# Kernel tuning notes

Measured on AMD Instinct MI355X. Metric: run time of the kernel, lower is better.

The kernel has to match this reference:

```python
import jax, jax.numpy as jnp
import numpy as np

GROUPS = 32
EPS = 1e-6


def group_norm(x, gamma, beta):
    b, c, h, w = x.shape
    xg = x.reshape(b, GROUPS, c // GROUPS, h, w)
    mean = xg.mean(axis=(2, 3, 4), keepdims=True)
    var = xg.var(axis=(2, 3, 4), keepdims=True)
    xn = (xg - mean) * jax.lax.rsqrt(var + EPS)
    xn = xn.reshape(b, c, h, w)
    return xn * gamma[None, :, None, None] + beta[None, :, None, None]


def conv1x1(x, w, b):
    # x: [B,C,H,W], w: [O,C], b: [O]
    return jnp.einsum('bchw,oc->bohw', x, w) + b[None, :, None, None]


def setup_inputs() -> dict:
    key = jax.random.key(0)
    ks = jax.random.split(key, 6)
    C = 512
    B, H, W = 2, 64, 64
    s = (C) ** -0.5  # fan-in style init scale for 1x1 convs
    return {
        'x': jax.random.normal(ks[0], (B, C, H, W), jnp.float32),
        'gn_gamma': jnp.ones((C,), jnp.float32),
        'gn_beta': jnp.zeros((C,), jnp.float32),
        'wq': jax.random.normal(ks[1], (C, C), jnp.float32) * s,
        'bq': jnp.zeros((C,), jnp.float32),
        'wk': jax.random.normal(ks[2], (C, C), jnp.float32) * s,
        'bk': jnp.zeros((C,), jnp.float32),
        'wv': jax.random.normal(ks[3], (C, C), jnp.float32) * s,
        'bv': jnp.zeros((C,), jnp.float32),
        'wo': jax.random.normal(ks[4], (C, C), jnp.float32) * s,
        'bo': jnp.zeros((C,), jnp.float32),
    }


def reference(x, gn_gamma, gn_beta, wq, bq, wk, bk, wv, bv, wo, bo):
    b, c, h, w = x.shape
    n = h * w
    h_ = group_norm(x, gn_gamma, gn_beta)
    q = conv1x1(h_, wq, bq).reshape(b, c, n)   # [B,C,N]
    k = conv1x1(h_, wk, bk).reshape(b, c, n)   # [B,C,N]
    v = conv1x1(h_, wv, bv).reshape(b, c, n)   # [B,C,N]
    scale = jnp.asarray(int(c) ** (-0.5), x.dtype)
    # scores[b, nq, nk] = sum_c q[b,c,nq] * k[b,c,nk]
    scores = jnp.einsum('bcn,bcm->bnm', q, k) * scale
    attn = jax.nn.softmax(scores, axis=2)      # softmax over keys
    # out[b,c,nq] = sum_m v[b,c,m] * attn[b,nq,m]
    out = jnp.einsum('bcm,bnm->bcn', v, attn).reshape(b, c, h, w)
    out = conv1x1(out, wo, bo)
    return x + out
```

## Files before the change

kernel.cpp:

```cpp
#include <hip/hip_runtime.h>

typedef unsigned short u16;
typedef __attribute__((ext_vector_type(8))) unsigned short ushort8;
typedef __attribute__((ext_vector_type(8))) short bf16x8;
typedef __attribute__((ext_vector_type(4))) float f32x4;

#define DEVINL __device__ __forceinline__

DEVINL float bf2f(u16 u){ union{unsigned i; float f;} v; v.i = ((unsigned)u) << 16; return v.f; }
DEVINL u16 f2bf(float f){
  unsigned x = __builtin_bit_cast(unsigned, f);
  x += 0x7fffu + ((x >> 16) & 1u);
  return (u16)(x >> 16);
}
DEVINL void gl_lds16(const void* g, void* l){
  __builtin_amdgcn_global_load_lds((const __attribute__((address_space(1))) unsigned*)g,
                                   (__attribute__((address_space(3))) unsigned*)l, 16, 0, 0);
}
template<int N> DEVINL void wait_vmcnt(){
  asm volatile("s_waitcnt vmcnt(%0)" :: "n"(N) : "memory");
}
DEVINL void hard_barrier(){
  asm volatile("" ::: "memory");
  __builtin_amdgcn_s_barrier();
  asm volatile("" ::: "memory");
}
DEVINL float wsum(float v){
  #pragma unroll
  for (int o = 32; o; o >>= 1) v += __shfl_xor(v, o, 64);
  return v;
}

__global__ __launch_bounds__(256) void cvt4b_k(const float* __restrict__ s0, const float* __restrict__ s1,
                 const float* __restrict__ s2, const float* __restrict__ s3,
                 const float* __restrict__ bq, const float* __restrict__ bk, const float* __restrict__ bv,
                 u16* __restrict__ wdst, float* __restrict__ bdst){
  if (blockIdx.x == 512){
    for (int j = threadIdx.x; j < 1536; j += 256)
      bdst[j] = (j < 512) ? bq[j] : (j < 1024) ? bk[j-512] : bv[j-1024];
    return;
  }
  const int g = blockIdx.x >> 7;
  const float* src = (g==0) ? s0 : (g==1) ? s1 : (g==2) ? s2 : s3;
  const int i = ((blockIdx.x & 127)*256 + threadIdx.x)*8;
  float4 f0 = *(const float4*)(src + i);
  float4 f1 = *(const float4*)(src + i + 4);
  ushort8 o;
  o[0]=f2bf(f0.x); o[1]=f2bf(f0.y); o[2]=f2bf(f0.z); o[3]=f2bf(f0.w);
  o[4]=f2bf(f1.x); o[5]=f2bf(f1.y); o[6]=f2bf(f1.z); o[7]=f2bf(f1.w);
  *(ushort8*)(wdst + g*262144 + i) = o;
}

__global__ __launch_bounds__(256) void reduce4_k(const u16* __restrict__ part,
                 const float* __restrict__ psum, u16* __restrict__ dst){
  __shared__ float invsh[4];
  const int t = threadIdx.x, w = t>>6, ln = t&63;
  const int row = blockIdx.x*4 + w;
  float s = psum[ln*8192 + blockIdx.y*4096 + row];
  s = wsum(s);
  if (ln == 0) invsh[w] = 1.f / s;
  __syncthreads();
  const int i = (blockIdx.x*256 + t)*8;
  const u16* p = part + (size_t)blockIdx.y*8388608;
  float a[8] = {};
  #pragma unroll
  for (int ks = 0; ks < 4; ++ks){
    ushort8 u = *(const ushort8*)(p + (size_t)ks*2097152 + i);
    #pragma unroll
    for (int j = 0; j < 8; ++j) a[j] += bf2f(u[j]);
  }
  const float iv = invsh[w];
  ushort8 o;
  #pragma unroll
  for (int j = 0; j < 8; ++j) o[j] = f2bf(a[j] * iv);
  *(ushort8*)(dst + (size_t)blockIdx.y*2097152 + i) = o;
}

__global__ __launch_bounds__(256) void gn_stats_k(const float* __restrict__ x, float* __restrict__ stats){
  __shared__ __align__(16) float red[8];
  const float* px = x + ((size_t)blockIdx.x << 16);
  const int t = threadIdx.x;
  float s = 0.f, ss = 0.f;
  for (int off = t*4; off < 65536; off += 1024){
    float4 u = *(const float4*)(px + off);
    s  += u.x + u.y + u.z + u.w;
    ss += u.x*u.x + u.y*u.y + u.z*u.z + u.w*u.w;
  }
  s = wsum(s); ss = wsum(ss);
  if ((t & 63) == 0){ red[t>>6] = s; red[4+(t>>6)] = ss; }
  __syncthreads();
  if (t == 0){
    float S1 = red[0]+red[1]+red[2]+red[3];
    float S2 = red[4]+red[5]+red[6]+red[7];
    float mean = S1 * (1.f/65536.f);
    float var  = S2 * (1.f/65536.f) - mean*mean;
    stats[2*blockIdx.x]   = mean;
    stats[2*blockIdx.x+1] = rsqrtf(var + 1e-6f);
  }
}

__global__ __launch_bounds__(256) void gn_apply_k(const float* __restrict__ x, const float* __restrict__ gamma,
                 const float* __restrict__ beta, const float* __restrict__ stats, u16* __restrict__ ht){
  __shared__ __align__(16) u16 tile[32*512];
  const int b = blockIdx.y, n0 = blockIdx.x*32, t = threadIdx.x;
  #pragma unroll
  for (int it = 0; it < 8; ++it){
    int c  = it*64 + (t>>2);
    int nn = (t&3)*8;
    const float* px = x + ((size_t)(b*512 + c) << 12) + n0 + nn;
    float4 u0 = *(const float4*)(px);
    float4 u1 = *(const float4*)(px + 4);
    float mean = stats[2*(b*32 + (c>>4))];
    float rstd = stats[2*(b*32 + (c>>4)) + 1];
    float ga = gamma[c], be = beta[c];
    float f[8] = {u0.x,u0.y,u0.z,u0.w,u1.x,u1.y,u1.z,u1.w};
    #pragma unroll
    for (int j = 0; j < 8; ++j)
      tile[(nn+j)*512 + c] = f2bf((f[j] - mean) * rstd * ga + be);
  }
  __syncthreads();
  const int rw = t>>3, sg = t&7;
  #pragma unroll
  for (int uu = 0; uu < 8; ++uu){
    ushort8 v = *(const ushort8*)(tile + rw*512 + sg*64 + uu*8);
    *(ushort8*)(ht + ((size_t)(b*4096 + n0 + rw) << 9) + sg*64 + uu*8) = v;
  }
}

template<bool EXPSUM>
__global__ __launch_bounds__(512) void gemm8_nt(
    const u16* __restrict__ A, const u16* __restrict__ Bt, u16* __restrict__ C,
    float* __restrict__ psum,
    int K, int lda, int ldb, int ldc, int zdiv,
    long long aStrB, long long aStr, long long bStrB, long long bStr,
    long long cStrB, long long cStr)
{
  extern __shared__ __align__(16) char smem[];
  const int z = blockIdx.z, z1 = z / zdiv, z2 = z % zdiv;
  A  += (size_t)aStrB*z1 + (size_t)aStr*z2;
  Bt += (size_t)bStrB*z1 + (size_t)bStr*z2;
  C  += (size_t)cStrB*z1 + (size_t)cStr*z2;
  const int nwg = gridDim.x*gridDim.y;
  int wg = blockIdx.y*gridDim.x + blockIdx.x;
  wg = (wg & 7)*(nwg >> 3) + (wg >> 3);
  const int m0 = (wg / gridDim.x)*256, n0 = (wg % gridDim.x)*256;

  const int t = threadIdx.x, wv = t>>6, ln = t&63;
  const int wm = wv>>2, wn = wv&3;
  const int lq = ln&15, lg = ln>>4;
  const int srow = ln>>2;
  const int sseg = (((ln&3) ^ ((srow>>1)&3)))*8;
  const int rslot = (lg ^ ((lq>>1)&3))*16;

  auto STAGE_A = [&](int u){
    char* base = smem + (u&3)*16384 + wv*1024;
    const u16* g = A + (size_t)(m0 + wv*16 + srow)*lda + u*32 + sseg;
    gl_lds16(g, base);
    gl_lds16(g + (size_t)128*lda, base + 8192);
  };
  auto STAGE_B = [&](int u){
    char* base = smem + 65536 + (u&3)*16384 + wv*1024;
    const u16* g = Bt + (size_t)(n0 + wv*16 + srow)*ldb + u*32 + sseg;
    gl_lds16(g, base);
    gl_lds16(g + (size_t)128*ldb, base + 8192);
  };
  auto LDA4 = [&](int u, int mh, bf16x8* a){
    const char* p = smem + (u&3)*16384 + (wm*128 + mh*64 + lq)*64 + rslot;
    #pragma unroll
    for (int i = 0; i < 4; ++i) a[i] = *(const bf16x8*)(p + i*1024);
  };
  auto LDB4 = [&](int u, bf16x8* b){
    const char* p = smem + 65536 + (u&3)*16384 + (wn*64 + lq)*64 + rslot;
    #pragma unroll
    for (int j = 0; j < 4; ++j) b[j] = *(const bf16x8*)(p + j*1024);
  };

  f32x4 acc[8][4] = {};
  auto MFMA16 = [&](bf16x8* a4, bf16x8* b4, int moff){
    __builtin_amdgcn_s_setprio(1);
    #pragma unroll
    for (int n = 0; n < 4; ++n)
      #pragma unroll
      for (int m = 0; m < 4; ++m)
        acc[moff+m][n] = __builtin_amdgcn_mfma_f32_16x16x32_bf16(a4[m], b4[n], acc[moff+m][n], 0, 0, 0);
    __builtin_amdgcn_s_setprio(0);
  };

  STAGE_A(0); STAGE_B(0); STAGE_A(1); STAGE_B(1); STAGE_A(2); STAGE_B(2);
  wait_vmcnt<8>();
  hard_barrier();
  const int T = K >> 6;
  for (int tt = 0; tt < T; ++tt){
    const int u0 = 2*tt, u1 = 2*tt + 1;
    bf16x8 a[4], b[4];
    LDA4(u0, 0, a); LDB4(u0, b);
    if (tt < T-1) STAGE_A(u0+3);
    hard_barrier();
    MFMA16(a, b, 0);
    hard_barrier();
    LDA4(u0, 1, a);
    if (tt < T-1) STAGE_B(u0+3);
    if (tt == T-1) wait_vmcnt<0>(); else wait_vmcnt<8>();
    hard_barrier();
    MFMA16(a, b, 4);
    hard_barrier();
    LDA4(u1, 0, a); LDB4(u1, b);
    if (tt < T-2) STAGE_A(u0+4);
    hard_barrier();
    MFMA16(a, b, 0);
    hard_barrier();
    LDA4(u1, 1, a);
    if (tt < T-2) STAGE_B(u0+4);
    if (tt == T-2)      wait_vmcnt<4>();
    else if (tt < T-2)  wait_vmcnt<8>();
    hard_barrier();
    MFMA16(a, b, 4);
    hard_barrier();
  }
  const int slice = EXPSUM ? ((n0 >> 8)*4 + wn) : 0;
  #pragma unroll
  for (int m = 0; m < 8; ++m)
    #pragma unroll
    for (int r2 = 0; r2 < 4; ++r2){
      const int mg = m0 + wm*128 + m*16 + lg*4 + r2;
      u16* cp = C + (size_t)mg*ldc + n0 + wn*64 + lq;
      if constexpr (EXPSUM){
        float e[4], rs = 0.f;
        #pragma unroll
        for (int n = 0; n < 4; ++n){ e[n] = __expf(acc[m][n][r2]); rs += e[n]; }
        rs += __shfl_xor(rs, 1, 64);
        rs += __shfl_xor(rs, 2, 64);
        rs += __shfl_xor(rs, 4, 64);
        rs += __shfl_xor(rs, 8, 64);
        if (lq == 0) psum[slice*8192 + z1*4096 + mg] = rs;
        #pragma unroll
        for (int n = 0; n < 4; ++n) cp[n*16] = f2bf(e[n]);
      } else {
        #pragma unroll
        for (int n = 0; n < 4; ++n) cp[n*16] = f2bf(acc[m][n][r2]);
      }
    }
}

__global__ __launch_bounds__(256) void qkv_k(
    const u16* __restrict__ Wstk, const u16* __restrict__ ht,
    const float* __restrict__ biases, u16* __restrict__ dstBase)
{
  __shared__ __align__(16) char smem[32768];
  char* smA0 = smem;
  char* smA1 = smem + 8192;
  char* smB0 = smem + 16384;
  char* smB1 = smem + 24576;
  const int z = blockIdx.z, mat = z >> 1, b = z & 1;
  const u16* A  = Wstk + mat*262144;
  const u16* Bt = ht + (size_t)b*2097152;
  const float* bias = biases + mat*512;
  const float oscale = (mat == 0) ? 0.044194173824159216f : 1.0f;
  u16* dst = dstBase + (size_t)mat*4194304 + (size_t)b*2097152;
  const int m0 = blockIdx.y*128, n0 = blockIdx.x*128;
  const int t = threadIdx.x, wv = t>>6, ln = t&63;
  const int wm = wv>>1, wn = wv&1;
  const int lq = ln&15, lg = ln>>4;
  const int srow = ln>>2;
  const int sseg = (((ln&3) ^ ((srow>>1)&3)))*8;
  const int rslot = (lg ^ ((lq>>1)&3))*16;
  f32x4 acc[4][4] = {};
  for (int kk = 0; kk < 512; kk += 64){
    __syncthreads();
    #pragma unroll
    for (int r = 0; r < 2; ++r){
      const int rr = r*64 + wv*16;
      const u16* pa = A  + (size_t)(m0 + rr + srow)*512 + kk + sseg;
      const u16* pb = Bt + (size_t)(n0 + rr + srow)*512 + kk + sseg;
      gl_lds16(pa,      smA0 + rr*64);
      gl_lds16(pa + 32, smA1 + rr*64);
      gl_lds16(pb,      smB0 + rr*64);
      gl_lds16(pb + 32, smB1 + rr*64);
    }
    __syncthreads();
    #pragma unroll
    for (int half = 0; half < 2; ++half){
      const char* pA = half ? smA1 : smA0;
      const char* pB = half ? smB1 : smB0;
      bf16x8 af[4], bfv[4];
      #pragma unroll
      for (int i = 0; i < 4; ++i) af[i]  = *(const bf16x8*)(pA + ((wm*64 + i*16 + lq)<<6) + rslot);
      #pragma unroll
      for (int j = 0; j < 4; ++j) bfv[j] = *(const bf16x8*)(pB + ((wn*64 + j*16 + lq)<<6) + rslot);
      #pragma unroll
      for (int i = 0; i < 4; ++i)
        #pragma unroll
        for (int j = 0; j < 4; ++j)
          acc[i][j] = __builtin_amdgcn_mfma_f32_16x16x32_bf16(af[i], bfv[j], acc[i][j], 0, 0, 0);
    }
  }
  if (mat == 2){
    #pragma unroll
    for (int i = 0; i < 4; ++i)
      #pragma unroll
      for (int r2 = 0; r2 < 4; ++r2){
        const int mg = m0 + wm*64 + i*16 + lg*4 + r2;
        float bv = bias[mg];
        #pragma unroll
        for (int j = 0; j < 4; ++j){
          const int ng = n0 + wn*64 + j*16 + lq;
          dst[(size_t)mg*4096 + ng] = f2bf(acc[i][j][r2] + bv);
        }
      }
  } else {
    __syncthreads();
    u16* ct = (u16*)smem;
    #pragma unroll
    for (int i = 0; i < 4; ++i)
      #pragma unroll
      for (int j = 0; j < 4; ++j)
        #pragma unroll
        for (int r2 = 0; r2 < 4; ++r2){
          const int ml = wm*64 + i*16 + lg*4 + r2;
          const int nl = wn*64 + j*16 + lq;
          ct[nl*128 + ml] = f2bf((acc[i][j][r2] + bias[m0 + ml]) * oscale);
        }
    __syncthreads();
    const int rw = t>>1, hf = (t&1)*64;
    #pragma unroll
    for (int u = 0; u < 8; ++u){
      *(ushort8*)(dst + (size_t)(n0 + rw)*512 + m0 + hf + u*8) =
          *(const ushort8*)(ct + rw*128 + hf + u*8);
    }
  }
}

template<bool TRANS_OUT, bool HAS_BIAS, bool HAS_RES, bool F32OUT>
__global__ __launch_bounds__(256) void gemm_nt(
    const u16* __restrict__ A, const u16* __restrict__ Bt,
    const float* __restrict__ bias, const float* __restrict__ res, void* __restrict__ Cw_,
    int K, int lda, int ldb, int ldc, int zdiv,
    long long aStrB, long long aStr, long long bStrB, long long bStr,
    long long cStrB, long long cStr, long long rStrB, float oscale)
{
  __shared__ __align__(16) char smem[32768];
  char* smA0 = smem;
  char* smA1 = smem + 8192;
  char* smB0 = smem + 16384;
  char* smB1 = smem + 24576;
  const int z = blockIdx.z;
  const int z1 = z / zdiv, z2 = z % zdiv;
  A  += (size_t)aStrB*z1 + (size_t)aStr*z2;
  Bt += (size_t)bStrB*z1 + (size_t)bStr*z2;
  u16*   Cw16 = (u16*)Cw_   + (size_t)cStrB*z1 + (size_t)cStr*z2;
  float* Cw32 = (float*)Cw_ + (size_t)cStrB*z1 + (size_t)cStr*z2;
  const float* resp = HAS_RES ? (res + (size_t)rStrB*z1) : nullptr;
  const int m0 = blockIdx.y*128, n0 = blockIdx.x*128;
  const int t = threadIdx.x, wv = t>>6, ln = t&63;
  const int wm = wv>>1, wn = wv&1;
  const int lq = ln&15, lg = ln>>4;
  const int srow = ln>>2;
  const int sseg = (((ln&3) ^ ((srow>>1)&3)))*8;
  const int rslot = (lg ^ ((lq>>1)&3))*16;
  f32x4 acc[4][4] = {};
  for (int kk = 0; kk < K; kk += 64){
    __syncthreads();
    #pragma unroll
    for (int r = 0; r < 2; ++r){
      const int rr = r*64 + wv*16;
      const u16* pa = A  + (size_t)(m0 + rr + srow)*lda + kk + sseg;
      const u16* pb = Bt + (size_t)(n0 + rr + srow)*ldb + kk + sseg;
      gl_lds16(pa,      smA0 + rr*64);
      gl_lds16(pa + 32, smA1 + rr*64);
      gl_lds16(pb,      smB0 + rr*64);
      gl_lds16(pb + 32, smB1 + rr*64);
    }
    __syncthreads();
    #pragma unroll
    for (int half = 0; half < 2; ++half){
      const char* pA = half ? smA1 : smA0;
      const char* pB = half ? smB1 : smB0;
      bf16x8 af[4], bfv[4];
      #pragma unroll
      for (int i = 0; i < 4; ++i) af[i]  = *(const bf16x8*)(pA + ((wm*64 + i*16 + lq)<<6) + rslot);
      #pragma unroll
      for (int j = 0; j < 4; ++j) bfv[j] = *(const bf16x8*)(pB + ((wn*64 + j*16 + lq)<<6) + rslot);
      #pragma unroll
      for (int i = 0; i < 4; ++i)
        #pragma unroll
        for (int j = 0; j < 4; ++j)
          acc[i][j] = __builtin_amdgcn_mfma_f32_16x16x32_bf16(af[i], bfv[j], acc[i][j], 0, 0, 0);
    }
  }
  if constexpr (!TRANS_OUT){
    #pragma unroll
    for (int i = 0; i < 4; ++i){
      #pragma unroll
      for (int r2 = 0; r2 < 4; ++r2){
        const int mg = m0 + wm*64 + i*16 + lg*4 + r2;
        float bv = HAS_BIAS ? bias[mg] : 0.f;
        #pragma unroll
        for (int j = 0; j < 4; ++j){
          const int ng = n0 + wn*64 + j*16 + lq;
          float v = (acc[i][j][r2] + bv) * oscale;
          if (HAS_RES) v += resp[(size_t)mg*ldc + ng];
          if constexpr (F32OUT) Cw32[(size_t)mg*ldc + ng] = v;
          else                  Cw16[(size_t)mg*ldc + ng] = f2bf(v);
        }
      }
    }
  } else {
    __syncthreads();
    u16* ct = (u16*)smem;
    #pragma unroll
    for (int i = 0; i < 4; ++i)
      #pragma unroll
      for (int j = 0; j < 4; ++j)
        #pragma unroll
        for (int r2 = 0; r2 < 4; ++r2){
          const int ml = wm*64 + i*16 + lg*4 + r2;
          const int nl = wn*64 + j*16 + lq;
          float v = acc[i][j][r2];
          if (HAS_BIAS) v += bias[m0 + ml];
          ct[nl*128 + ml] = f2bf(v * oscale);
        }
    __syncthreads();
    const int rw = t>>1, hf = (t&1)*64;
    #pragma unroll
    for (int u = 0; u < 8; ++u){
      *(ushort8*)(Cw16 + (size_t)(n0 + rw)*ldc + m0 + hf + u*8) =
          *(const ushort8*)(ct + rw*128 + hf + u*8);
    }
  }
}

extern "C" void kernel_launch(void* const* d_in, const int* in_sizes, int n_in,
                              void* d_out, int out_size, void* d_ws, size_t ws_size,
                              hipStream_t stream)
{
  const float* x   = (const float*)d_in[0];
  const float* gam = (const float*)d_in[1];
  const float* bet = (const float*)d_in[2];
  const float* wq  = (const float*)d_in[3];
  const float* bq  = (const float*)d_in[4];
  const float* wk  = (const float*)d_in[5];
  const float* bk  = (const float*)d_in[6];
  const float* wvp = (const float*)d_in[7];
  const float* bv  = (const float*)d_in[8];
  const float* wo  = (const float*)d_in[9];
  const float* bo  = (const float*)d_in[10];
  float* out = (float*)d_out;

  char* w = (char*)d_ws;
  float* stats   = (float*)w;
  float* psum    = (float*)(w + 4096);
  float* biasQKV = (float*)(w + 2134016);
  u16* wqb  = (u16*)(w + (size_t)4194304);
  u16* wob  = wqb + 3*262144;
  u16* Qt   = wqb + 4*262144;
  u16* Kt   = Qt + 4194304;
  u16* Vb   = Kt + 4194304;
  u16* attT = Vb + 4194304;
  u16* Sbuf = attT + 4194304;
  u16* part = Sbuf + 33554432;
  u16* ht   = (u16*)d_out;

  const long long NC = 4096LL*512, NN = 4096LL*4096;

  cvt4b_k<<<dim3(513), dim3(256), 0, stream>>>(wq, wk, wvp, wo, bq, bk, bv, wqb, biasQKV);
  gn_stats_k<<<dim3(64), dim3(256), 0, stream>>>(x, stats);
  gn_apply_k<<<dim3(128,2), dim3(256), 0, stream>>>(x, gam, bet, stats, ht);
  qkv_k<<<dim3(32,4,6), dim3(256), 0, stream>>>(wqb, ht, biasQKV, Qt);
  gemm8_nt<true><<<dim3(16,16,2), dim3(512), 131072, stream>>>(
      Qt, Kt, Sbuf, psum, 512, 512, 512, 4096, 1, NC, 0, NC, 0, NN, 0);
  gemm8_nt<false><<<dim3(2,16,8), dim3(512), 131072, stream>>>(
      Sbuf, Vb, part, nullptr, 1024, 4096, 4096, 512, 4,
      NN, 1024, NC, 1024, 8388608, 2097152);
  reduce4_k<<<dim3(1024,2), dim3(256), 0, stream>>>(part, psum, attT);
  gemm_nt<false, true, true, true><<<dim3(32,4,2), dim3(256), 0, stream>>>(
      wob, attT, bo, x, out, 512, 512, 512, 4096, 1, 0,0, NC,0, NC,0, NC, 1.0f);
}
```

Measured before the change: 187.1 us.

## Shrink GEMM LDS to double buffering and split PV GEMM K eight ways

The 256x256 bf16 GEMM drops its 4-stage LDS ring and hand-scheduled two-step loop in favour of a 2-stage double buffer with a simple per-k-step loop, halving dynamic LDS from 128KB to 64KB. With less LDS per block, two blocks could fit per CU. The attention-times-V GEMM now splits K into 8 chunks of 512 instead of 4 of 1024, doubling its grid, and the reduction kernel sums 8 bf16 partials. The trade-off is less prefetch depth with a full vmcnt(0) wait every step, plus double the partial-buffer traffic and an extra bf16 rounding stage in the reduction.

New measurement: 197.4 us. 1.06x slower.

```diff
diff --git a/kernel.cpp b/kernel.cpp
--- a/kernel.cpp
+++ b/kernel.cpp
@@ -51,7 +51,7 @@
   *(ushort8*)(wdst + g*262144 + i) = o;
 }
 
-__global__ __launch_bounds__(256) void reduce4_k(const u16* __restrict__ part,
+__global__ __launch_bounds__(256) void reduce8_k(const u16* __restrict__ part,
                  const float* __restrict__ psum, u16* __restrict__ dst){
   __shared__ float invsh[4];
   const int t = threadIdx.x, w = t>>6, ln = t&63;
@@ -61,10 +61,10 @@
   if (ln == 0) invsh[w] = 1.f / s;
   __syncthreads();
   const int i = (blockIdx.x*256 + t)*8;
-  const u16* p = part + (size_t)blockIdx.y*8388608;
+  const u16* p = part + (size_t)blockIdx.y*16777216;
   float a[8] = {};
   #pragma unroll
-  for (int ks = 0; ks < 4; ++ks){
+  for (int ks = 0; ks < 8; ++ks){
     ushort8 u = *(const ushort8*)(p + (size_t)ks*2097152 + i);
     #pragma unroll
     for (int j = 0; j < 8; ++j) a[j] += bf2f(u[j]);
@@ -153,24 +153,24 @@
   const int rslot = (lg ^ ((lq>>1)&3))*16;
 
   auto STAGE_A = [&](int u){
-    char* base = smem + (u&3)*16384 + wv*1024;
+    char* base = smem + (u&1)*16384 + wv*1024;
     const u16* g = A + (size_t)(m0 + wv*16 + srow)*lda + u*32 + sseg;
     gl_lds16(g, base);
     gl_lds16(g + (size_t)128*lda, base + 8192);
   };
   auto STAGE_B = [&](int u){
-    char* base = smem + 65536 + (u&3)*16384 + wv*1024;
+    char* base = smem + 32768 + (u&1)*16384 + wv*1024;
     const u16* g = Bt + (size_t)(n0 + wv*16 + srow)*ldb + u*32 + sseg;
     gl_lds16(g, base);
     gl_lds16(g + (size_t)128*ldb, base + 8192);
   };
   auto LDA4 = [&](int u, int mh, bf16x8* a){
-    const char* p = smem + (u&3)*16384 + (wm*128 + mh*64 + lq)*64 + rslot;
+    const char* p = smem + (u&1)*16384 + (wm*128 + mh*64 + lq)*64 + rslot;
     #pragma unroll
     for (int i = 0; i < 4; ++i) a[i] = *(const bf16x8*)(p + i*1024);
   };
   auto LDB4 = [&](int u, bf16x8* b){
-    const char* p = smem + 65536 + (u&3)*16384 + (wn*64 + lq)*64 + rslot;
+    const char* p = smem + 32768 + (u&1)*16384 + (wn*64 + lq)*64 + rslot;
     #pragma unroll
     for (int j = 0; j < 4; ++j) b[j] = *(const bf16x8*)(p + j*1024);
   };
@@ -186,36 +186,17 @@
     __builtin_amdgcn_s_setprio(0);
   };
 
-  STAGE_A(0); STAGE_B(0); STAGE_A(1); STAGE_B(1); STAGE_A(2); STAGE_B(2);
-  wait_vmcnt<8>();
-  hard_barrier();
-  const int T = K >> 6;
-  for (int tt = 0; tt < T; ++tt){
-    const int u0 = 2*tt, u1 = 2*tt + 1;
-    bf16x8 a[4], b[4];
-    LDA4(u0, 0, a); LDB4(u0, b);
-    if (tt < T-1) STAGE_A(u0+3);
+  STAGE_A(0); STAGE_B(0);
+  const int U = K >> 5;
+  for (int u = 0; u < U; ++u){
+    wait_vmcnt<0>();
     hard_barrier();
-    MFMA16(a, b, 0);
-    hard_barrier();
-    LDA4(u0, 1, a);
-    if (tt < T-1) STAGE_B(u0+3);
-    if (tt == T-1) wait_vmcnt<0>(); else wait_vmcnt<8>();
-    hard_barrier();
-    MFMA16(a, b, 4);
-    hard_barrier();
-    LDA4(u1, 0, a); LDB4(u1, b);
-    if (tt < T-2) STAGE_A(u0+4);
-    hard_barrier();
-    MFMA16(a, b, 0);
-    hard_barrier();
-    LDA4(u1, 1, a);
-    if (tt < T-2) STAGE_B(u0+4);
-    if (tt == T-2)      wait_vmcnt<4>();
-    else if (tt < T-2)  wait_vmcnt<8>();
-    hard_barrier();
-    MFMA16(a, b, 4);
-    hard_barrier();
+    bf16x8 a0[4], a1[4], b[4];
+    LDA4(u, 0, a0); LDB4(u, b);
+    if (u + 1 < U){ STAGE_A(u+1); STAGE_B(u+1); }
+    MFMA16(a0, b, 0);
+    LDA4(u, 1, a1);
+    MFMA16(a1, b, 4);
   }
   const int slice = EXPSUM ? ((n0 >> 8)*4 + wn) : 0;
   #pragma unroll
@@ -466,12 +447,12 @@
   gn_stats_k<<<dim3(64), dim3(256), 0, stream>>>(x, stats);
   gn_apply_k<<<dim3(128,2), dim3(256), 0, stream>>>(x, gam, bet, stats, ht);
   qkv_k<<<dim3(32,4,6), dim3(256), 0, stream>>>(wqb, ht, biasQKV, Qt);
-  gemm8_nt<true><<<dim3(16,16,2), dim3(512), 131072, stream>>>(
+  gemm8_nt<true><<<dim3(16,16,2), dim3(512), 65536, stream>>>(
       Qt, Kt, Sbuf, psum, 512, 512, 512, 4096, 1, NC, 0, NC, 0, NN, 0);
-  gemm8_nt<false><<<dim3(2,16,8), dim3(512), 131072, stream>>>(
-      Sbuf, Vb, part, nullptr, 1024, 4096, 4096, 512, 4,
-      NN, 1024, NC, 1024, 8388608, 2097152);
-  reduce4_k<<<dim3(1024,2), dim3(256), 0, stream>>>(part, psum, attT);
+  gemm8_nt<false><<<dim3(2,16,16), dim3(512), 65536, stream>>>(
+      Sbuf, Vb, part, nullptr, 512, 4096, 4096, 512, 8,
+      NN, 512, NC, 512, 16777216, 2097152);
+  reduce8_k<<<dim3(1024,2), dim3(256), 0, stream>>>(part, psum, attT);
   gemm_nt<false, true, true, true><<<dim3(32,4,2), dim3(256), 0, stream>>>(
       wob, attT, bo, x, out, 512, 512, 512, 4096, 1, 0,0, NC,0, NC,0, NC, 1.0f);
 }
```
